# Optimization experiments

Hardware: AMD Instinct MI355X
Metric: run time of the kernel (lower is better)

The kernel has to match this reference:

```python
import jax, jax.numpy as jnp
import numpy as np

B, T, C = 2, 2048, 1024
H = 16
D = C // H  # head_dim = 64
EPS = 1e-06
MAX_SEQ = 2048


def make_rotary(dim, max_seq_len, base=10000):
    inv_freq = 1.0 / (base ** (jnp.arange(0, dim, 2, dtype=jnp.float32) / dim))
    pos = jnp.arange(max_seq_len, dtype=jnp.float32)
    sinusoid = jnp.einsum('i,j->ij', pos, inv_freq)  # (S, dim//2)
    return jnp.sin(sinusoid), jnp.cos(sinusoid)


def apply_rotary(x, sin, cos):
    # x: (B, T, H, D); sin/cos: (MAX_SEQ, D//2)
    t = x.shape[1]
    s = sin[:t][:, None, :]  # (T,1,D//2) broadcasts over B and H
    c = cos[:t][:, None, :]
    d = x.shape[-1]
    x1, x2 = x[..., :d // 2], x[..., d // 2:]
    return jnp.concatenate([x1 * c - x2 * s, x2 * c + x1 * s], axis=-1)


def yat_dense(x, kernel, bias, alpha, eps=EPS):
    # Yat layer: squared dot product over squared euclidean distance.
    dot = x @ kernel                                   # (..., out)
    x_sq = jnp.sum(x * x, axis=-1, keepdims=True)      # (..., 1)
    k_sq = jnp.sum(kernel * kernel, axis=0)            # (out,)
    dist = x_sq + k_sq - 2.0 * dot
    y = (dot * dot) / (dist + eps)
    out_f = kernel.shape[1]
    scale = (jnp.sqrt(jnp.float32(out_f)) / jnp.log(1.0 + jnp.float32(out_f))) ** alpha
    return y * scale + bias


def setup_inputs() -> dict:
    key = jax.random.key(0)
    ks = jax.random.split(key, 7)
    x = jax.random.normal(ks[0], (B, T, C), dtype=jnp.float32)
    mask = jnp.tril(jnp.ones((T, T), dtype=bool))[None].repeat(B, axis=0)  # (B,T,T) causal
    s = 1.0 / np.sqrt(C)
    w_attn = jax.random.normal(ks[1], (C, 3 * C), dtype=jnp.float32) * s
    b_attn = jnp.zeros((3 * C,), dtype=jnp.float32)
    a_attn = jnp.ones((1,), dtype=jnp.float32)
    w_proj = jax.random.normal(ks[2], (C, C), dtype=jnp.float32) * s
    b_proj = jnp.zeros((C,), dtype=jnp.float32)
    a_proj = jnp.ones((1,), dtype=jnp.float32)
    return {"x": x, "mask": mask, "w_attn": w_attn, "b_attn": b_attn,
            "a_attn": a_attn, "w_proj": w_proj, "b_proj": b_proj, "a_proj": a_proj}


def reference(x, mask, w_attn, b_attn, a_attn, w_proj, b_proj, a_proj):
    b, t, c = x.shape
    sin, cos = make_rotary(D, MAX_SEQ)
    qkv = yat_dense(x, w_attn, b_attn, a_attn)          # (B,T,3C)
    qkv = qkv.reshape(b, t, 3, H, D)
    q, k, v = jnp.moveaxis(qkv, 2, 0)                   # each (B,T,H,D)
    q = apply_rotary(q, sin, cos)
    k = apply_rotary(k, sin, cos)
    # heads-major layout for attention
    q = q.transpose(0, 2, 1, 3)                          # (B,H,T,D)
    k = k.transpose(0, 2, 1, 3)
    v = v.transpose(0, 2, 1, 3)
    scale = jnp.sqrt(jnp.float32(D))
    attn = jnp.einsum('bhqd,bhkd->bhqk', q, k) / scale   # (B,H,T,T)
    m = mask[:, None, :, :]                              # (B,1,T,T)
    attn = jnp.where(m, attn, jnp.finfo(jnp.float32).min)
    attn = jax.nn.softmax(attn, axis=-1)
    # dropout is identity in deterministic/eval mode
    out = jnp.einsum('bhqk,bhkd->bhqd', attn, v)         # (B,H,T,D)
    out = out.transpose(0, 2, 1, 3).reshape(b, t, c)     # (B,T,C)
    out = yat_dense(out, w_proj, b_proj, a_proj)
    return out
```

## Files before the change

### kernel.cpp

```cpp
#include <hip/hip_runtime.h>
#include <math.h>

#define TSEQ  2048
#define BATCH 2
#define NH    16
#define HD    64
#define CDIM  1024
#define N3C   3072
#define EPSY  1e-6f

typedef unsigned short u16;
typedef unsigned int u32;
typedef __attribute__((ext_vector_type(8))) short bf16x8;
typedef __attribute__((ext_vector_type(4))) float f32x4;

#define MFMA16(a, b, c) __builtin_amdgcn_mfma_f32_16x16x32_bf16(a, b, c, 0, 0, 0)

__device__ __forceinline__ u16 f2bf(float f) {
    unsigned u = __float_as_uint(f);
    return (u16)((u + 0x7fffu + ((u >> 16) & 1u)) >> 16);
}
__device__ __forceinline__ float bf2f(u16 h) {
    return __uint_as_float(((unsigned)h) << 16);
}
__device__ __forceinline__ u32 cvtpk_bf16(float lo, float hi) {
    u32 r;
    asm("v_cvt_pk_bf16_f32 %0, %1, %2" : "=v"(r) : "v"(lo), "v"(hi));
    return r;
}
__device__ __forceinline__ void gload16(const void* g, void* l) {
    __builtin_amdgcn_global_load_lds(
        (const __attribute__((address_space(1))) unsigned int*)g,
        (__attribute__((address_space(3))) unsigned int*)l, 16, 0, 0);
}

__global__ __launch_bounds__(256) void prep_kernel(
    const float* __restrict__ x, const float* __restrict__ wa,
    const float* __restrict__ wp, u16* __restrict__ Ahi,
    u16* __restrict__ Wthi, u16* __restrict__ Wphi,
    float* __restrict__ ksq, float* __restrict__ xsq,
    float* __restrict__ osq, float2* __restrict__ ropeSC) {
    __shared__ float smem[64 * 68];
    int bid = blockIdx.x, tid = threadIdx.x;

    if (bid < 4096) {
        int lane = tid & 63, wv = tid >> 6;
        size_t base = (size_t)bid * CDIM + tid * 4;
        float4 v = *(const float4*)(x + base);
        ushort4 hi;
        hi.x = f2bf(v.x); hi.y = f2bf(v.y); hi.z = f2bf(v.z); hi.w = f2bf(v.w);
        *(ushort4*)(Ahi + base) = hi;
        float s = v.x * v.x + v.y * v.y + v.z * v.z + v.w * v.w;
        #pragma unroll
        for (int off = 32; off; off >>= 1) s += __shfl_down(s, off, 64);
        if (lane == 0) smem[wv] = s;
        __syncthreads();
        if (tid == 0) xsq[bid] = smem[0] + smem[1] + smem[2] + smem[3];
    } else if (bid < 5120) {
        const float* W; u16* Whi; int K, N, bx, by;
        if (bid < 4864) {
            int t = bid - 4096; W = wa; Whi = Wthi; K = CDIM; N = N3C;
            bx = t % 48; by = t / 48;
        } else {
            int t = bid - 4864; W = wp; Whi = Wphi; K = CDIM; N = CDIM;
            bx = t % 16; by = t / 16;
        }
        int k0 = by * 64, n0 = bx * 64;
        int r = tid >> 4, c4 = (tid & 15) * 4;
        #pragma unroll
        for (int i = 0; i < 4; ++i) {
            int k = k0 + r + i * 16;
            float4 v = *(const float4*)(W + (size_t)k * N + n0 + c4);
            *(float4*)&smem[(r + i * 16) * 68 + c4] = v;
        }
        __syncthreads();
        int n = tid >> 4, k4 = (tid & 15) * 4;
        #pragma unroll
        for (int i = 0; i < 4; ++i) {
            int nn = n + i * 16;
            ushort4 hi;
            hi.x = f2bf(smem[(k4 + 0) * 68 + nn]);
            hi.y = f2bf(smem[(k4 + 1) * 68 + nn]);
            hi.z = f2bf(smem[(k4 + 2) * 68 + nn]);
            hi.w = f2bf(smem[(k4 + 3) * 68 + nn]);
            *(ushort4*)(Whi + (size_t)(n0 + nn) * K + k0 + k4) = hi;
        }
    } else if (bid < 5184) {
        int b2 = bid - 5120;
        int c = tid & 63, kq = tid >> 6;
        const float* W; int N, col, outoff;
        if (b2 < 48) { W = wa; N = N3C;  col = b2 * 64 + c;        outoff = 0;   }
        else         { W = wp; N = CDIM; col = (b2 - 48) * 64 + c; outoff = N3C; }
        float s = 0.f;
        int i0 = kq * 256;
        #pragma unroll 4
        for (int i = i0; i < i0 + 256; ++i) {
            float v = W[(size_t)i * N + col];
            s = fmaf(v, v, s);
        }
        smem[tid] = s;
        __syncthreads();
        if (kq == 0)
            ksq[outoff + col] = smem[c] + smem[64 + c] + smem[128 + c] + smem[192 + c];
    } else {
        int idx = (bid - 5184) * 256 + tid;
        if (idx < BATCH * TSEQ) osq[idx] = 0.f;
        int t = idx >> 5, j = idx & 31;
        float inv = exp2f(-(float)j * 0.4152410118609203f);
        float ang = (float)t * inv;
        ropeSC[idx] = make_float2(cosf(ang), sinf(ang));
    }
}

__global__ __launch_bounds__(256, 4) void gemm1_fused(
    const u16* __restrict__ Ah, const u16* __restrict__ Bh,
    const float* __restrict__ bias, const float* __restrict__ rowsq,
    const float* __restrict__ colsq, const float* __restrict__ alphap,
    const float2* __restrict__ ropeSC,
    u16* __restrict__ Qb, u16* __restrict__ Kb, u16* __restrict__ Vt) {
    constexpr int BK = 32;
    const int K = CDIM;
    __shared__ u16 Ash[2][128 * BK], Bsh[2][128 * BK];
    int tid = threadIdx.x;
    int lane = tid & 63, wv = tid >> 6;
    int quad = lane >> 4, l15 = lane & 15;
    int wr = wv >> 1, wc = wv & 1;
    int bm = blockIdx.y * 128, bn = blockIdx.x * 128;
    int rsub = lane >> 2;
    int lc8 = (lane & 3) * 8;
    int gc8 = (((lane & 3) - (rsub >> 1)) & 3) * 8;
    int pf8 = ((quad + (l15 >> 1)) & 3) * 8;

    f32x4 acc[4][4];
    #pragma unroll
    for (int i = 0; i < 4; ++i)
        #pragma unroll
        for (int j = 0; j < 4; ++j) acc[i][j] = (f32x4){0.f, 0.f, 0.f, 0.f};

    auto STAGE = [&](int buf, int kt) {
        #pragma unroll
        for (int i = 0; i < 2; ++i) {
            int r = i * 64 + wv * 16 + rsub;
            gload16(Ah + (size_t)(bm + r) * K + kt + gc8, &Ash[buf][r * BK + lc8]);
            gload16(Bh + (size_t)(bn + r) * K + kt + gc8, &Bsh[buf][r * BK + lc8]);
        }
    };

    STAGE(0, 0);
    __syncthreads();
    int cur = 0;

    for (int kt = 0; kt < K; kt += BK) {
        if (kt + BK < K) STAGE(cur ^ 1, kt + BK);
        bf16x8 fah[4], fbh[4];
        #pragma unroll
        for (int i = 0; i < 4; ++i)
            fah[i] = *(const bf16x8*)&Ash[cur][(wr * 64 + i * 16 + l15) * BK + pf8];
        #pragma unroll
        for (int j = 0; j < 4; ++j)
            fbh[j] = *(const bf16x8*)&Bsh[cur][(wc * 64 + j * 16 + l15) * BK + pf8];
        #pragma unroll
        for (int i = 0; i < 4; ++i)
            #pragma unroll
            for (int j = 0; j < 4; ++j)
                acc[i][j] = MFMA16(fah[i], fbh[j], acc[i][j]);
        __syncthreads();
        cur ^= 1;
    }

    float alpha = alphap[0];
    float scale = powf(sqrtf((float)N3C) / logf(1.0f + (float)N3C), alpha);
    int segc0 = bn + wc * 64;
    int seg = segc0 >> 10;
    int h = (segc0 >> 6) & 15;
    int bglob = bm >> 11;
    int bh = bglob * NH + h;

    if (seg < 2) {
        u16* dst = (seg == 0) ? Qb : Kb;
        float qs = (seg == 0) ? 0.125f : 1.0f;
        #pragma unroll
        for (int i = 0; i < 4; ++i) {
            int tb = bm + wr * 64 + i * 16 + quad * 4;
            #pragma unroll
            for (int r = 0; r < 4; ++r) {
                int row = tb + r;
                int t = row & (TSEQ - 1);
                float rs = rowsq[row];
                float y[4];
                #pragma unroll
                for (int j = 0; j < 4; ++j) {
                    int col = segc0 + j * 16 + l15;
                    float dot = acc[i][j][r];
                    float dist = rs + colsq[col] - 2.0f * dot + EPSY;
                    y[j] = dot * dot / dist * scale + bias[col];
                }
                float2 sc0 = ropeSC[t * 32 + l15];
                float2 sc1 = ropeSC[t * 32 + 16 + l15];
                float c0 = sc0.x, s0 = sc0.y, c1 = sc1.x, s1 = sc1.y;
                size_t ob = ((size_t)bh * TSEQ + t) * HD;
                dst[ob + l15]      = f2bf((y[0] * c0 - y[2] * s0) * qs);
                dst[ob + 16 + l15] = f2bf((y[1] * c1 - y[3] * s1) * qs);
                dst[ob + 32 + l15] = f2bf((y[2] * c0 + y[0] * s0) * qs);
                dst[ob + 48 + l15] = f2bf((y[3] * c1 + y[1] * s1) * qs);
            }
        }
    } else {
        #pragma unroll
        for (int i = 0; i < 4; ++i) {
            int tb = bm + wr * 64 + i * 16 + quad * 4;
            int t0 = tb & (TSEQ - 1);
            #pragma unroll
            for (int j = 0; j < 4; ++j) {
                int col = segc0 + j * 16 + l15;
                int d = j * 16 + l15;
                float cs = colsq[col], bi = bias[col];
                ushort4 pk;
                u16* pp = (u16*)&pk;
                #pragma unroll
                for (int r = 0; r < 4; ++r) {
                    float dot = acc[i][j][r];
                    float dist = rowsq[tb + r] + cs - 2.0f * dot + EPSY;
                    pp[r] = f2bf(dot * dot / dist * scale + bi);
                }
                *(ushort4*)(Vt + ((size_t)bh * HD + d) * TSEQ + t0) = pk;
            }
        }
    }
}

__global__ __launch_bounds__(256, 4) void gemm_yat_mfma(
    const u16* __restrict__ Ah, const u16* __restrict__ Bh,
    const float* __restrict__ bias, const float* __restrict__ rowsq,
    const float* __restrict__ colsq, const float* __restrict__ alphap,
    float* __restrict__ outp, int M, int N, int K, float outf) {
    constexpr int BM = 128, BN = 64, BK = 32;
    __shared__ u16 Ash[2][BM * BK], Bsh[2][BN * BK];
    int tid = threadIdx.x;
    int lane = tid & 63, wv = tid >> 6;
    int quad = lane >> 4, l15 = lane & 15;
    int bm = blockIdx.y * BM, bn = blockIdx.x * BN;
    int rsub = lane >> 2;
    int lc8 = (lane & 3) * 8;
    int gc8 = (((lane & 3) - (rsub >> 1)) & 3) * 8;
    int pf8 = ((quad + (l15 >> 1)) & 3) * 8;

    f32x4 acc[2][4];
    #pragma unroll
    for (int i = 0; i < 2; ++i)
        #pragma unroll
        for (int j = 0; j < 4; ++j) acc[i][j] = (f32x4){0.f, 0.f, 0.f, 0.f};

    auto STAGE = [&](int buf, int kt) {
        #pragma unroll
        for (int i = 0; i < 2; ++i) {
            int r = i * 64 + wv * 16 + rsub;
            gload16(Ah + (size_t)(bm + r) * K + kt + gc8, &Ash[buf][r * BK + lc8]);
        }
        {
            int r = wv * 16 + rsub;
            gload16(Bh + (size_t)(bn + r) * K + kt + gc8, &Bsh[buf][r * BK + lc8]);
        }
    };

    STAGE(0, 0);
    __syncthreads();
    int cur = 0;

    for (int kt = 0; kt < K; kt += BK) {
        if (kt + BK < K) STAGE(cur ^ 1, kt + BK);
        bf16x8 fah[2], fbh[4];
        #pragma unroll
        for (int i = 0; i < 2; ++i)
            fah[i] = *(const bf16x8*)&Ash[cur][(wv * 32 + i * 16 + l15) * BK + pf8];
        #pragma unroll
        for (int j = 0; j < 4; ++j)
            fbh[j] = *(const bf16x8*)&Bsh[cur][(j * 16 + l15) * BK + pf8];
        #pragma unroll
        for (int i = 0; i < 2; ++i)
            #pragma unroll
            for (int j = 0; j < 4; ++j)
                acc[i][j] = MFMA16(fah[i], fbh[j], acc[i][j]);
        __syncthreads();
        cur ^= 1;
    }

    float alpha = alphap[0];
    float scale = powf(sqrtf(outf) / logf(1.0f + outf), alpha);
    #pragma unroll
    for (int j = 0; j < 4; ++j) {
        int col = bn + j * 16 + l15;
        float cs = colsq[col], bi = bias[col];
        #pragma unroll
        for (int i = 0; i < 2; ++i) {
            #pragma unroll
            for (int r = 0; r < 4; ++r) {
                int row = bm + wv * 32 + i * 16 + quad * 4 + r;
                float dot = acc[i][j][r];
                float dist = rowsq[row] + cs - 2.0f * dot + EPSY;
                outp[(size_t)row * N + col] = dot * dot / dist * scale + bi;
            }
        }
    }
}

__global__ __launch_bounds__(256) void attn_mfma(
    const u16* __restrict__ Qb, const u16* __restrict__ Kb,
    const u16* __restrict__ Vt, u16* __restrict__ Chi,
    float* __restrict__ osq) {
    __shared__ u16 Ksh[2][64 * 64];
    __shared__ u16 Vsh[2][64 * 64];
    int tid = threadIdx.x;
    int lane = tid & 63, wv = tid >> 6;
    int quad = lane >> 4, l15 = lane & 15;
    int bh = blockIdx.x;
    int b = bh >> 4, h = bh & 15;
    const u16* Qh = Qb + (size_t)bh * TSEQ * HD;
    const u16* Kh = Kb + (size_t)bh * TSEQ * HD;
    const u16* Vh = Vt + (size_t)bh * HD * TSEQ;
    const f32x4 zf = {0.f, 0.f, 0.f, 0.f};

    int qb = 31 - blockIdx.y;
    int qw = qb * 64 + wv * 16;
    bf16x8 bq0 = *(const bf16x8*)(Qh + (size_t)(qw + l15) * HD + quad * 8);
    bf16x8 bq1 = *(const bf16x8*)(Qh + (size_t)(qw + l15) * HD + 32 + quad * 8);

    f32x4 o[4] = {zf, zf, zf, zf};
    float l = 0.f;

    auto STAGE = [&](int buf, int kt) {
        int k0s = kt * 64;
        #pragma unroll
        for (int p = 0; p < 2; ++p) {
            int lin = p * 256 + tid;
            int rowi = lin >> 3, ch = lin & 7;
            int gk = (ch + rowi) & 7;
            gload16(Kh + (size_t)(k0s + rowi) * HD + gk * 8, &Ksh[buf][lin * 8]);
            gload16(Vh + (size_t)rowi * TSEQ + k0s + gk * 8, &Vsh[buf][lin * 8]);
        }
    };

    STAGE(0, 0);
    __syncthreads();
    int cur = 0;

    for (int kt = 0; kt <= qb; ++kt) {
        int k0 = kt * 64;
        if (kt < qb) STAGE(cur ^ 1, kt + 1);
        const u16* Kc = Ksh[cur];
        const u16* Vc = Vsh[cur];

        f32x4 st[4];
        __builtin_amdgcn_s_setprio(1);
        #pragma unroll
        for (int mt = 0; mt < 4; ++mt) {
            int key = mt * 16 + l15;
            bf16x8 a0 = *(const bf16x8*)&Kc[key * 64 + ((quad - key) & 7) * 8];
            bf16x8 a1 = *(const bf16x8*)&Kc[key * 64 + ((4 + quad - key) & 7) * 8];
            st[mt] = MFMA16(a0, bq0, zf);
            st[mt] = MFMA16(a1, bq1, st[mt]);
        }
        __builtin_amdgcn_s_setprio(0);
        if (kt == qb) {
            int q = qw + l15;
            #pragma unroll
            for (int mt = 0; mt < 4; ++mt)
                #pragma unroll
                for (int r = 0; r < 4; ++r)
                    if (k0 + mt * 16 + quad * 4 + r > q) st[mt][r] = -1e30f;
        }
        u32 pp[4][2];
        #pragma unroll
        for (int mt = 0; mt < 4; ++mt) {
            float p0 = __expf(st[mt][0]);
            float p1 = __expf(st[mt][1]);
            float p2 = __expf(st[mt][2]);
            float p3 = __expf(st[mt][3]);
            l += (p0 + p1) + (p2 + p3);
            pp[mt][0] = cvtpk_bf16(p0, p1);
            pp[mt][1] = cvtpk_bf16(p2, p3);
        }
        #pragma unroll
        for (int s = 0; s < 2; ++s) {
            u32 bw[4];
            #pragma unroll
            for (int w = 0; w < 4; ++w) {
                int srcl = (((quad & 1) * 2 + (w >> 1)) << 4) + l15;
                u32 vlo = (u32)__shfl((int)pp[2 * s][w & 1], srcl, 64);
                u32 vhi = (u32)__shfl((int)pp[2 * s + 1][w & 1], srcl, 64);
                bw[w] = (quad & 2) ? vhi : vlo;
            }
            bf16x8 bfr;
            *(u32*)&((short*)&bfr)[0] = bw[0];
            *(u32*)&((short*)&bfr)[2] = bw[1];
            *(u32*)&((short*)&bfr)[4] = bw[2];
            *(u32*)&((short*)&bfr)[6] = bw[3];
            __builtin_amdgcn_s_setprio(1);
            #pragma unroll
            for (int dt = 0; dt < 4; ++dt) {
                int d = dt * 16 + l15;
                bf16x8 av = *(const bf16x8*)&Vc[d * 64 + ((s * 4 + quad - d) & 7) * 8];
                o[dt] = MFMA16(av, bfr, o[dt]);
            }
            __builtin_amdgcn_s_setprio(0);
        }
        __syncthreads();
        cur ^= 1;
    }

    l += __shfl_xor(l, 16, 64);
    l += __shfl_xor(l, 32, 64);
    float inv = 1.0f / l;
    int row = (b << 11) + qw + l15;
    float ss = 0.f;
    #pragma unroll
    for (int dt = 0; dt < 4; ++dt) {
        float v0 = o[dt][0] * inv, v1 = o[dt][1] * inv;
        float v2 = o[dt][2] * inv, v3 = o[dt][3] * inv;
        ss += v0 * v0 + v1 * v1 + v2 * v2 + v3 * v3;
        uint2 pk2;
        pk2.x = cvtpk_bf16(v0, v1);
        pk2.y = cvtpk_bf16(v2, v3);
        *(uint2*)(Chi + (size_t)row * CDIM + h * HD + dt * 16 + quad * 4) = pk2;
    }
    ss += __shfl_xor(ss, 16, 64);
    ss += __shfl_xor(ss, 32, 64);
    if (quad == 0) atomicAdd(osq + row, ss);
}

extern "C" void kernel_launch(void* const* d_in, const int* in_sizes, int n_in,
                              void* d_out, int out_size, void* d_ws, size_t ws_size,
                              hipStream_t stream) {
    const float* x      = (const float*)d_in[0];
    const float* w_attn = (const float*)d_in[2];
    const float* b_attn = (const float*)d_in[3];
    const float* a_attn = (const float*)d_in[4];
    const float* w_proj = (const float*)d_in[5];
    const float* b_proj = (const float*)d_in[6];
    const float* a_proj = (const float*)d_in[7];
    float* outp = (float*)d_out;

    char* ws = (char*)d_ws;
    float* ksq = (float*)(ws);
    float* xsq = (float*)(ws + 16384);
    float* osq = (float*)(ws + 32768);
    char* pA  = ws + 65536;
    u16* Ahi = (u16*)pA;
    u16* Chi = (u16*)pA;
    char* pWt = pA + 16777216;
    u16* Wthi = (u16*)pWt;
    char* pWp = pWt + 6291456;
    u16* Wphi = (u16*)pWp;
    char* pQ = pWp + 2097152;
    u16* Qb = (u16*)pQ;
    u16* Kb = (u16*)(pQ + 8388608);
    u16* Vt = (u16*)(pQ + 16777216);
    float2* ropeSC = (float2*)(pQ + 25165824);

    prep_kernel<<<5440, 256, 0, stream>>>(
        x, w_attn, w_proj, Ahi, Wthi, Wphi, ksq, xsq, osq, ropeSC);
    gemm1_fused<<<dim3(N3C / 128, (BATCH * TSEQ) / 128), 256, 0, stream>>>(
        Ahi, Wthi, b_attn, xsq, ksq, a_attn, ropeSC, Qb, Kb, Vt);
    attn_mfma<<<dim3(BATCH * NH, 32), 256, 0, stream>>>(Qb, Kb, Vt, Chi, osq);
    gemm_yat_mfma<<<dim3(CDIM / 64, (BATCH * TSEQ) / 128), 256, 0, stream>>>(
        Chi, Wphi, b_proj, osq, ksq + N3C, a_proj, outp,
        BATCH * TSEQ, CDIM, CDIM, (float)CDIM);
}
```

Measured before the change: 230.3 us.

## Enlarge attention query block to 128 rows, use exp2 and permlane shuffles

The attention kernel now runs 512-thread blocks that each cover 128 queries across 8 waves, so every staged K/V tile in shared memory serves twice as many queries. Waves whose queries lie entirely before a key tile skip its compute but still join the barrier. The softmax uses hardware exp2 with log2(e) folded into the Q scale. The P-fragment shuffles are replaced by permlane32_swap plus ds_swizzle. The larger blocks may leave some waves idle and reduce occupancy.

```diff
diff --git a/kernel.cpp b/kernel.cpp
--- a/kernel.cpp
+++ b/kernel.cpp
@@ -11,6 +11,7 @@
 
 typedef unsigned short u16;
 typedef unsigned int u32;
+typedef __attribute__((ext_vector_type(2))) unsigned int u32x2;
 typedef __attribute__((ext_vector_type(8))) short bf16x8;
 typedef __attribute__((ext_vector_type(4))) float f32x4;
 
@@ -19,9 +20,6 @@
 __device__ __forceinline__ u16 f2bf(float f) {
     unsigned u = __float_as_uint(f);
     return (u16)((u + 0x7fffu + ((u >> 16) & 1u)) >> 16);
-}
-__device__ __forceinline__ float bf2f(u16 h) {
-    return __uint_as_float(((unsigned)h) << 16);
 }
 __device__ __forceinline__ u32 cvtpk_bf16(float lo, float hi) {
     u32 r;
@@ -178,7 +176,7 @@
 
     if (seg < 2) {
         u16* dst = (seg == 0) ? Qb : Kb;
-        float qs = (seg == 0) ? 0.125f : 1.0f;
+        float qs = (seg == 0) ? 0.18033688011112043f : 1.0f;
         #pragma unroll
         for (int i = 0; i < 4; ++i) {
             int tb = bm + wr * 64 + i * 16 + quad * 4;
@@ -304,7 +302,7 @@
     }
 }
 
-__global__ __launch_bounds__(256) void attn_mfma(
+__global__ __launch_bounds__(512) void attn_mfma(
     const u16* __restrict__ Qb, const u16* __restrict__ Kb,
     const u16* __restrict__ Vt, u16* __restrict__ Chi,
     float* __restrict__ osq) {
@@ -313,6 +311,7 @@
     int tid = threadIdx.x;
     int lane = tid & 63, wv = tid >> 6;
     int quad = lane >> 4, l15 = lane & 15;
+    const bool oddq = (quad & 1) != 0;
     int bh = blockIdx.x;
     int b = bh >> 4, h = bh & 15;
     const u16* Qh = Qb + (size_t)bh * TSEQ * HD;
@@ -320,8 +319,9 @@
     const u16* Vh = Vt + (size_t)bh * HD * TSEQ;
     const f32x4 zf = {0.f, 0.f, 0.f, 0.f};
 
-    int qb = 31 - blockIdx.y;
-    int qw = qb * 64 + wv * 16;
+    int qbb = 15 - blockIdx.y;
+    int qw = qbb * 128 + wv * 16;
+    int NT = 2 * qbb + 2;
     bf16x8 bq0 = *(const bf16x8*)(Qh + (size_t)(qw + l15) * HD + quad * 8);
     bf16x8 bq1 = *(const bf16x8*)(Qh + (size_t)(qw + l15) * HD + 32 + quad * 8);
 
@@ -330,79 +330,81 @@
 
     auto STAGE = [&](int buf, int kt) {
         int k0s = kt * 64;
-        #pragma unroll
-        for (int p = 0; p < 2; ++p) {
-            int lin = p * 256 + tid;
-            int rowi = lin >> 3, ch = lin & 7;
-            int gk = (ch + rowi) & 7;
-            gload16(Kh + (size_t)(k0s + rowi) * HD + gk * 8, &Ksh[buf][lin * 8]);
-            gload16(Vh + (size_t)rowi * TSEQ + k0s + gk * 8, &Vsh[buf][lin * 8]);
-        }
+        int rowi = tid >> 3, ch = tid & 7;
+        int gk = (ch + rowi) & 7;
+        gload16(Kh + (size_t)(k0s + rowi) * HD + gk * 8, &Ksh[buf][tid * 8]);
+        gload16(Vh + (size_t)rowi * TSEQ + k0s + gk * 8, &Vsh[buf][tid * 8]);
     };
 
     STAGE(0, 0);
     __syncthreads();
     int cur = 0;
 
-    for (int kt = 0; kt <= qb; ++kt) {
+    for (int kt = 0; kt < NT; ++kt) {
         int k0 = kt * 64;
-        if (kt < qb) STAGE(cur ^ 1, kt + 1);
-        const u16* Kc = Ksh[cur];
-        const u16* Vc = Vsh[cur];
-
-        f32x4 st[4];
-        __builtin_amdgcn_s_setprio(1);
-        #pragma unroll
-        for (int mt = 0; mt < 4; ++mt) {
-            int key = mt * 16 + l15;
-            bf16x8 a0 = *(const bf16x8*)&Kc[key * 64 + ((quad - key) & 7) * 8];
-            bf16x8 a1 = *(const bf16x8*)&Kc[key * 64 + ((4 + quad - key) & 7) * 8];
-            st[mt] = MFMA16(a0, bq0, zf);
-            st[mt] = MFMA16(a1, bq1, st[mt]);
-        }
-        __builtin_amdgcn_s_setprio(0);
-        if (kt == qb) {
-            int q = qw + l15;
-            #pragma unroll
-            for (int mt = 0; mt < 4; ++mt)
+        if (kt + 1 < NT) STAGE(cur ^ 1, kt + 1);
+        if (k0 <= qw + 15) {
+            const u16* Kc = Ksh[cur];
+            const u16* Vc = Vsh[cur];
+
+            f32x4 st[4];
+            __builtin_amdgcn_s_setprio(1);
+            #pragma unroll
+            for (int mt = 0; mt < 4; ++mt) {
+                int key = mt * 16 + l15;
+                bf16x8 a0 = *(const bf16x8*)&Kc[key * 64 + ((quad - key) & 7) * 8];
+                bf16x8 a1 = *(const bf16x8*)&Kc[key * 64 + ((4 + quad - key) & 7) * 8];
+                st[mt] = MFMA16(a0, bq0, zf);
+                st[mt] = MFMA16(a1, bq1, st[mt]);
+            }
+            __builtin_amdgcn_s_setprio(0);
+            if (k0 + 63 > qw) {
+                int q = qw + l15;
                 #pragma unroll
-                for (int r = 0; r < 4; ++r)
-                    if (k0 + mt * 16 + quad * 4 + r > q) st[mt][r] = -1e30f;
-        }
-        u32 pp[4][2];
-        #pragma unroll
-        for (int mt = 0; mt < 4; ++mt) {
-            float p0 = __expf(st[mt][0]);
-            float p1 = __expf(st[mt][1]);
-            float p2 = __expf(st[mt][2]);
-            float p3 = __expf(st[mt][3]);
-            l += (p0 + p1) + (p2 + p3);
-            pp[mt][0] = cvtpk_bf16(p0, p1);
-            pp[mt][1] = cvtpk_bf16(p2, p3);
-        }
-        #pragma unroll
-        for (int s = 0; s < 2; ++s) {
-            u32 bw[4];
-            #pragma unroll
-            for (int w = 0; w < 4; ++w) {
-                int srcl = (((quad & 1) * 2 + (w >> 1)) << 4) + l15;
-                u32 vlo = (u32)__shfl((int)pp[2 * s][w & 1], srcl, 64);
-                u32 vhi = (u32)__shfl((int)pp[2 * s + 1][w & 1], srcl, 64);
-                bw[w] = (quad & 2) ? vhi : vlo;
-            }
-            bf16x8 bfr;
-            *(u32*)&((short*)&bfr)[0] = bw[0];
-            *(u32*)&((short*)&bfr)[2] = bw[1];
-            *(u32*)&((short*)&bfr)[4] = bw[2];
-            *(u32*)&((short*)&bfr)[6] = bw[3];
-            __builtin_amdgcn_s_setprio(1);
-            #pragma unroll
-            for (int dt = 0; dt < 4; ++dt) {
-                int d = dt * 16 + l15;
-                bf16x8 av = *(const bf16x8*)&Vc[d * 64 + ((s * 4 + quad - d) & 7) * 8];
-                o[dt] = MFMA16(av, bfr, o[dt]);
-            }
-            __builtin_amdgcn_s_setprio(0);
+                for (int mt = 0; mt < 4; ++mt)
+                    #pragma unroll
+                    for (int r = 0; r < 4; ++r)
+                        if (k0 + mt * 16 + quad * 4 + r > q) st[mt][r] = -1e30f;
+            }
+            u32 pp[4][2];
+            #pragma unroll
+            for (int mt = 0; mt < 4; ++mt) {
+                float p0 = __builtin_amdgcn_exp2f(st[mt][0]);
+                float p1 = __builtin_amdgcn_exp2f(st[mt][1]);
+                float p2 = __builtin_amdgcn_exp2f(st[mt][2]);
+                float p3 = __builtin_amdgcn_exp2f(st[mt][3]);
+                l += (p0 + p1) + (p2 + p3);
+                pp[mt][0] = cvtpk_bf16(p0, p1);
+                pp[mt][1] = cvtpk_bf16(p2, p3);
+            }
+            #pragma unroll
+            for (int s = 0; s < 2; ++s) {
+                u32x2 r0 = __builtin_amdgcn_permlane32_swap(
+                    pp[2 * s][0], pp[2 * s + 1][0], false, false);
+                u32 sA0 = (u32)__builtin_amdgcn_ds_swizzle((int)r0.x, 0x401F);
+                u32 sB0 = (u32)__builtin_amdgcn_ds_swizzle((int)r0.y, 0x401F);
+                u32x2 r1 = __builtin_amdgcn_permlane32_swap(
+                    pp[2 * s][1], pp[2 * s + 1][1], false, false);
+                u32 sA1 = (u32)__builtin_amdgcn_ds_swizzle((int)r1.x, 0x401F);
+                u32 sB1 = (u32)__builtin_amdgcn_ds_swizzle((int)r1.y, 0x401F);
+                u32 bw0 = oddq ? sB0 : r0.x;
+                u32 bw1 = oddq ? sB1 : r1.x;
+                u32 bw2 = oddq ? r0.y : sA0;
+                u32 bw3 = oddq ? r1.y : sA1;
+                bf16x8 bfr;
+                *(u32*)&((short*)&bfr)[0] = bw0;
+                *(u32*)&((short*)&bfr)[2] = bw1;
+                *(u32*)&((short*)&bfr)[4] = bw2;
+                *(u32*)&((short*)&bfr)[6] = bw3;
+                __builtin_amdgcn_s_setprio(1);
+                #pragma unroll
+                for (int dt = 0; dt < 4; ++dt) {
+                    int d = dt * 16 + l15;
+                    bf16x8 av = *(const bf16x8*)&Vc[d * 64 + ((s * 4 + quad - d) & 7) * 8];
+                    o[dt] = MFMA16(av, bfr, o[dt]);
+                }
+                __builtin_amdgcn_s_setprio(0);
+            }
         }
         __syncthreads();
         cur ^= 1;
@@ -461,7 +463,7 @@
         x, w_attn, w_proj, Ahi, Wthi, Wphi, ksq, xsq, osq, ropeSC);
     gemm1_fused<<<dim3(N3C / 128, (BATCH * TSEQ) / 128), 256, 0, stream>>>(
         Ahi, Wthi, b_attn, xsq, ksq, a_attn, ropeSC, Qb, Kb, Vt);
-    attn_mfma<<<dim3(BATCH * NH, 32), 256, 0, stream>>>(Qb, Kb, Vt, Chi, osq);
+    attn_mfma<<<dim3(BATCH * NH, 16), 512, 0, stream>>>(Qb, Kb, Vt, Chi, osq);
     gemm_yat_mfma<<<dim3(CDIM / 64, (BATCH * TSEQ) / 128), 256, 0, stream>>>(
         Chi, Wphi, b_proj, osq, ksq + N3C, a_proj, outp,
         BATCH * TSEQ, CDIM, CDIM, (float)CDIM);
```

After: 225.6 us. 1.02x faster.
